# Kernel tuning notes

Measured on AMD Instinct MI355X. Metric: run time of the kernel, lower is better.

Reference implementation:

```python
import jax, jax.numpy as jnp
import numpy as np

CX, CY, FX, FY = 334.081, 169.808, 460.585, 460.268
EPS = 1e-07
T_ITER = 1000
MIN_POINTS = 5000
H, W, B = 360, 640, 2


def _point_cloud(depth_img):
    # depth_img: [C,H,W]; channel 2 if C==3 else channel 0
    depth = depth_img[2] if depth_img.shape[0] == 3 else depth_img[0]
    rows, cols = depth.shape
    c = jnp.arange(cols, dtype=depth.dtype)[None, :]
    r = jnp.arange(rows, dtype=depth.dtype)[:, None]
    valid = (depth > 0) & (depth < 65535)
    nanv = jnp.float32(jnp.nan)
    z = jnp.where(valid, depth / 1000.0, nanv)
    x = jnp.where(valid, z * (c - CX) / FX, nanv)
    y = jnp.where(valid, z * (r - CY) / FY, nanv)
    pcd = jnp.stack([x.ravel(), y.ravel(), z.ravel()], axis=1)  # [N,3]
    return pcd, valid.ravel()


def setup_inputs() -> dict:
    key = jax.random.key(0)
    k1, k2 = jax.random.split(key)
    fake = jax.random.uniform(k1, (B, 1, H, W), dtype=jnp.float32)
    real = jax.random.uniform(k2, (B, 1, H, W), dtype=jnp.float32)
    return {"fake": fake, "real": real, "epoch": 5, "show_image": 0}


def _forward(fake, real, epoch):
    real_pcd, vr = _point_cloud(real[0])
    fake_pcd, vf = _point_cloud(fake[0])
    real_pcd = real_pcd * 1000.0
    fake_pcd = fake_pcd * 1000.0
    # pcd[pcd==0] = eps  (NaN==0 is False, NaNs preserved)
    real_pcd = jnp.where(real_pcd == 0, EPS, real_pcd)
    fake_pcd = jnp.where(fake_pcd == 0, EPS, fake_pcd)

    # combined validity mask (real-valid then fake-valid filtering chain)
    m = vr & vf
    cnt = jnp.maximum(jnp.sum(m), 1)

    def sel(v, fill):
        return jnp.where(m, v, fill)

    def mrmse(a, b):
        d = sel(a, 0.0) - sel(b, 0.0)
        return jnp.sqrt(jnp.sum(d * d) / cnt)

    lossX = mrmse(real_pcd[:, 0], fake_pcd[:, 0])
    lossY = mrmse(real_pcd[:, 1], fake_pcd[:, 1])
    lossZ = mrmse(real_pcd[:, 2], fake_pcd[:, 2])
    dlog = jnp.log(jnp.abs(sel(real_pcd[:, 2], 1.0))) - jnp.log(jnp.abs(sel(fake_pcd[:, 2], 1.0)))
    RMSE_log = 10000.0 * jnp.sqrt(jnp.sum(jnp.where(m, dlog * dlog, 0.0)) / cnt)
    loss17 = RMSE_log * jnp.abs(10.0 * (3.0 - jnp.exp(lossX) - jnp.exp(lossY) - jnp.exp(lossZ)))

    # ---- batched RANSAC plane fit on normalized fake cloud ----
    nan_cloud = jnp.where(jnp.isnan(fake_pcd), 0.0, fake_pcd)
    pts = nan_cloud / jnp.max(nan_cloud)  # [N,3]
    N = pts.shape[0]
    thresh = jnp.maximum(jnp.float32(0.025 - 0.001 * epoch), jnp.float32(0.005))

    rkey = jax.random.key(42)
    idx = jax.random.randint(rkey, (T_ITER, 3), 0, N)  # 3 sample points per trial
    p = pts[idx]  # [T,3,3]
    vA = p[:, 1] - p[:, 0]
    vB = p[:, 2] - p[:, 0]
    nrm = jnp.cross(vA, vB)
    nrm = nrm / jnp.linalg.norm(nrm, axis=1, keepdims=True)  # unit normals [T,3]
    kk = -jnp.sum(nrm * p[:, 1], axis=1)  # plane offsets [T]
    dist = pts @ nrm.T + kk[None, :]  # [N,T], |n|=1 so no extra divide
    inl = jnp.abs(dist) <= thresh  # [N,T]
    counts = jnp.sum(inl, axis=0)  # [T]
    # keep first trial with strictly-largest count among counts > minPoints
    score = jnp.where(counts > MIN_POINTS, counts, -1)
    best = jnp.argmax(score)
    a, b, c, d = nrm[best, 0], nrm[best, 1], nrm[best, 2], kk[best]
    inlier_mask = inl[:, best]  # [N]

    # translation/rotation were built via torch.tensor(...) -> detached in torch
    trans = jax.lax.stop_gradient(jnp.stack([jnp.zeros(()), jnp.zeros(()), d / c]))
    n2 = a * a + b * b + c * c
    cos_t = c / jnp.sqrt(n2)
    sin_t = jnp.sqrt((a * a + b * b) / n2)
    sab = jnp.sqrt(a * a + b * b)
    u1 = b / sab
    u2 = -a / sab
    R = jnp.stack([
        jnp.stack([cos_t + u1 * u1 * (1 - cos_t), u1 * u2 * (1 - cos_t), u2 * sin_t]),
        jnp.stack([u1 * u2 * (1 - cos_t), cos_t + u2 * u2 * (1 - cos_t), -u1 * sin_t]),
        jnp.stack([-u2 * sin_t, u1 * sin_t, cos_t]),
    ])
    Rt = jax.lax.stop_gradient(R).T  # torch transposes before matmul

    plane_pts = pts + trans
    zc = (plane_pts @ Rt)[:, 2]  # rotated z for all points; inliers selected by mask
    icnt = jnp.maximum(jnp.sum(inlier_mask), 1)
    zmax = jnp.max(jnp.where(inlier_mask, zc, -jnp.inf))
    zmin = jnp.min(jnp.where(inlier_mask, zc, jnp.inf))
    below = jnp.sum(jnp.where(inlier_mask, jnp.abs(zc - zmax), 0.0)) / icnt
    above = jnp.sum(jnp.where(inlier_mask, jnp.abs(zc - zmin), 0.0)) / icnt
    above = jnp.where(above == 0, jnp.float32(1e-07), above)
    plane_mean_dist_grad = 1000.0 * (above + below)

    loss_curv = loss17 + plane_mean_dist_grad
    delta = jnp.stack([RMSE_log, lossX, lossY, lossZ, plane_mean_dist_grad, loss17])
    return delta, loss_curv


def reference(fake, real, epoch, show_image):
    del show_image  # unused in the loss math
    return _forward(fake, real, epoch)
```

## Files before the change

### kernel.cpp

```cpp
#include <hip/hip_runtime.h>

namespace {

typedef float v2f __attribute__((ext_vector_type(2)));

constexpr int kW = 640;
constexpr unsigned kSpan = 230400u;
constexpr int kB1 = 900;
constexpr int kB3 = 1024;
constexpr int kPPB3 = 225;
constexpr int kB5 = 900;
constexpr unsigned kPoison = 0xAAAAAAAAu;

constexpr size_t kOffMaxv    = 0;
constexpr size_t kOffL17     = 8;
constexpr size_t kOffSel     = 16;
constexpr size_t kOffC3      = 320;
constexpr size_t kOffC5      = 384;
constexpr size_t kOffPlanes  = 512;
constexpr size_t kOffSP      = 512 + 16384;
constexpr size_t kOffZP      = kOffSP + 43200;
constexpr size_t kOffPartial = kOffZP + 28800;
constexpr size_t kOffPts     = kOffPartial + (size_t)kB3 * 256 * 4;

__device__ __forceinline__ void ast64(unsigned long long* p, unsigned long long v) {
  __hip_atomic_store(p, v, __ATOMIC_RELAXED, __HIP_MEMORY_SCOPE_AGENT);
}
__device__ __forceinline__ unsigned long long ald64(const unsigned long long* p) {
  return __hip_atomic_load(p, __ATOMIC_RELAXED, __HIP_MEMORY_SCOPE_AGENT);
}
__device__ __forceinline__ void ast32(unsigned* p, unsigned v) {
  __hip_atomic_store(p, v, __ATOMIC_RELAXED, __HIP_MEMORY_SCOPE_AGENT);
}
__device__ __forceinline__ unsigned ald32(const unsigned* p) {
  return __hip_atomic_load(p, __ATOMIC_RELAXED, __HIP_MEMORY_SCOPE_AGENT);
}

__device__ __forceinline__ unsigned rotl32(unsigned v, int r) {
  return (v << r) | (v >> (32 - r));
}

__device__ __forceinline__ void threefry(unsigned c0, unsigned c1,
                                         unsigned& o0, unsigned& o1) {
  const unsigned ks0 = 0u, ks1 = 42u, ks2 = 0x1BD11BDAu ^ 0u ^ 42u;
  unsigned x0 = c0 + ks0, x1 = c1 + ks1;
#define TFR(r) { x0 += x1; x1 = rotl32(x1, (r)); x1 ^= x0; }
  TFR(13) TFR(15) TFR(26) TFR(6)
  x0 += ks1; x1 += ks2 + 1u;
  TFR(17) TFR(29) TFR(16) TFR(24)
  x0 += ks2; x1 += ks0 + 2u;
  TFR(13) TFR(15) TFR(26) TFR(6)
  x0 += ks0; x1 += ks1 + 3u;
  TFR(17) TFR(29) TFR(16) TFR(24)
  x0 += ks1; x1 += ks2 + 4u;
  TFR(13) TFR(15) TFR(26) TFR(6)
  x0 += ks2; x1 += ks0 + 5u;
#undef TFR
  o0 = x0; o1 = x1;
}

__device__ __forceinline__ void pix_coords(float d, int row, int col, bool& valid,
                                           float& x, float& y, float& z) {
  valid = (d > 0.0f) && (d < 65535.0f);
  float z0 = d / 1000.0f;
  float x0 = z0 * ((float)col - 334.081f) / 460.585f;
  float y0 = z0 * ((float)row - 169.808f) / 460.268f;
  x = x0 * 1000.0f;
  y = y0 * 1000.0f;
  z = z0 * 1000.0f;
  if (x == 0.0f) x = 1e-7f;
  if (y == 0.0f) y = 1e-7f;
  if (z == 0.0f) z = 1e-7f;
}

__device__ __forceinline__ void make_pt(float d, int row, int col, float maxv,
                                        float& x, float& y, float& z) {
  bool v; float a, b, c;
  pix_coords(d, row, col, v, a, b, c);
  x = (v ? a : 0.f) / maxv;
  y = (v ? b : 0.f) / maxv;
  z = (v ? c : 0.f) / maxv;
}

__device__ __forceinline__ float get_thresh(int ep) {
  return (float)fmax(0.025 - 0.001 * (double)ep, 0.005);
}

__global__ __launch_bounds__(256) void k_stats(const float* __restrict__ fake,
                                               const float* __restrict__ real,
                                               char* __restrict__ ws) {
  int* maxvBits = (int*)(ws + kOffMaxv);
  double* sp = (double*)(ws + kOffSP);
  float4* ptsraw = (float4*)(ws + kOffPts);

  const int b = blockIdx.x, t = threadIdx.x;
  const int lane = t & 63, wid = t >> 6;

  __shared__ double sD0[4], sD1[4], sD2[4], sD3[4];
  __shared__ int sI0[4];
  __shared__ float sF0[4];

  int i = b * 256 + t;
  int row = i / kW, col = i - row * kW;
  bool vr, vf; float rx, ry, rz, fx, fy, fz;
  pix_coords(real[i], row, col, vr, rx, ry, rz);
  pix_coords(fake[i], row, col, vf, fx, fy, fz);
  ptsraw[i] = make_float4(vf ? fx : 0.f, vf ? fy : 0.f, vf ? fz : 0.f, 0.f);
  double dx2 = 0, dy2 = 0, dz2 = 0, dl2 = 0; int cc = 0;
  if (vr && vf) {
    float ddx = rx - fx, ddy = ry - fy, ddz = rz - fz;
    dx2 = (double)ddx * (double)ddx;
    dy2 = (double)ddy * (double)ddy;
    dz2 = (double)ddz * (double)ddz;
    double dl = log(fabs((double)rz)) - log(fabs((double)fz));
    dl2 = dl * dl;
    cc = 1;
  }
  float mx = vf ? fmaxf(fmaxf(fx, fy), fz) : 0.0f;
  for (int o = 32; o; o >>= 1) {
    dx2 += __shfl_down(dx2, o); dy2 += __shfl_down(dy2, o);
    dz2 += __shfl_down(dz2, o); dl2 += __shfl_down(dl2, o);
    cc += __shfl_down(cc, o);
    mx = fmaxf(mx, __shfl_down(mx, o));
  }
  if (lane == 0) { sD0[wid]=dx2; sD1[wid]=dy2; sD2[wid]=dz2; sD3[wid]=dl2;
                   sI0[wid]=cc; sF0[wid]=mx; }
  __syncthreads();
  if (t == 0) {
    double* e = sp + (size_t)b * 6;
    e[0] = sD0[0]+sD0[1]+sD0[2]+sD0[3];
    e[1] = sD1[0]+sD1[1]+sD1[2]+sD1[3];
    e[2] = sD2[0]+sD2[1]+sD2[2]+sD2[3];
    e[3] = sD3[0]+sD3[1]+sD3[2]+sD3[3];
    e[4] = (double)(sI0[0]+sI0[1]+sI0[2]+sI0[3]);
    float bm = fmaxf(fmaxf(sF0[0], sF0[1]), fmaxf(sF0[2], sF0[3]));
    atomicMax(maxvBits, (int)__float_as_uint(bm));
  }
}

__global__ __launch_bounds__(256) void k_planes_scalars(const float* __restrict__ fake,
                                                        float* __restrict__ out,
                                                        char* __restrict__ ws) {
  const int* maxvBits = (const int*)(ws + kOffMaxv);
  double* loss17p = (double*)(ws + kOffL17);
  unsigned* selkeyp = (unsigned*)(ws + kOffSel);
  float4* planes = (float4*)(ws + kOffPlanes);
  const double* sp = (const double*)(ws + kOffSP);

  const int t = threadIdx.x;
  const int lane = t & 63, wid = t >> 6;

  if (blockIdx.x == 16) {
    __shared__ double sD0[4], sD1[4], sD2[4], sD3[4];
    __shared__ int sI0[4];
    double gx = 0, gy = 0, gz = 0, gl = 0; int gc = 0;
    for (int r = t; r < kB1; r += 256) {
      const double* e = sp + (size_t)r * 6;
      gx += e[0]; gy += e[1]; gz += e[2]; gl += e[3];
      gc += (int)e[4];
    }
    for (int o = 32; o; o >>= 1) {
      gx += __shfl_down(gx, o); gy += __shfl_down(gy, o);
      gz += __shfl_down(gz, o); gl += __shfl_down(gl, o);
      gc += __shfl_down(gc, o);
    }
    if (lane == 0) { sD0[wid]=gx; sD1[wid]=gy; sD2[wid]=gz; sD3[wid]=gl; sI0[wid]=gc; }
    __syncthreads();
    if (t == 0) {
      double SX = sD0[0]+sD0[1]+sD0[2]+sD0[3];
      double SY = sD1[0]+sD1[1]+sD1[2]+sD1[3];
      double SZ = sD2[0]+sD2[1]+sD2[2]+sD2[3];
      double SL = sD3[0]+sD3[1]+sD3[2]+sD3[3];
      int CN = sI0[0]+sI0[1]+sI0[2]+sI0[3];
      double cntd = (CN > 0) ? (double)CN : 1.0;
      double lossX = sqrt(SX / cntd);
      double lossY = sqrt(SY / cntd);
      double lossZ = sqrt(SZ / cntd);
      double rmse_log = 10000.0 * sqrt(SL / cntd);
      double loss17 = rmse_log * fabs(10.0 * (3.0 - exp(lossX) - exp(lossY) - exp(lossZ)));
      *loss17p = loss17;
      *selkeyp = 0u;
      out[0] = (float)rmse_log;
      out[1] = (float)lossX;
      out[2] = (float)lossY;
      out[3] = (float)lossZ;
      out[5] = (float)loss17;
    }
  } else {
    const float maxv = __uint_as_float((unsigned)*maxvBits);
    __shared__ float sX[192], sY[192], sZ[192];
    if (t < 192) {
      int j = t / 3;
      int v = t - j * 3;
      int pid = blockIdx.x * 64 + j;
      if (pid < 1000) {
        unsigned p = 3u * (unsigned)pid + (unsigned)v;
        unsigned o0, o1;
        threefry(p, p + 3000u, o0, o1);
        unsigned idx = o1 % kSpan;
        int row = (int)(idx / kW), col = (int)idx - row * kW;
        float x, y, z;
        make_pt(fake[idx], row, col, maxv, x, y, z);
        sX[t] = x; sY[t] = y; sZ[t] = z;
      }
    }
    __syncthreads();
    if (t < 64) {
      int pid = blockIdx.x * 64 + t;
      if (pid < 1000) {
        float px[3], py[3], pz[3];
#pragma unroll
        for (int v = 0; v < 3; v++) {
          px[v] = sX[3 * t + v]; py[v] = sY[3 * t + v]; pz[v] = sZ[3 * t + v];
        }
        float ax = px[1]-px[0], ay = py[1]-py[0], az = pz[1]-pz[0];
        float bx = px[2]-px[0], by = py[2]-py[0], bz = pz[2]-pz[0];
        float nx = ay*bz - az*by;
        float ny = az*bx - ax*bz;
        float nz = ax*by - ay*bx;
        float nn = sqrtf(nx*nx + ny*ny + nz*nz);
        nx /= nn; ny /= nn; nz /= nn;
        float kk = -(nx*px[1] + ny*py[1] + nz*pz[1]);
        planes[pid] = make_float4(nx, ny, nz, kk);
      } else {
        planes[pid] = make_float4(0.f, 0.f, 0.f, 3e38f);
      }
    }
  }
}

__global__ __launch_bounds__(256) void k_count(const int* __restrict__ epoch,
                                               char* __restrict__ ws) {
  unsigned* selkeyp = (unsigned*)(ws + kOffSel);
  unsigned* ctr = (unsigned*)(ws + kOffC3);
  const float4* planes = (const float4*)(ws + kOffPlanes);
  unsigned* partial = (unsigned*)(ws + kOffPartial);
  const float4* ptsraw = (const float4*)(ws + kOffPts);

  const int b = blockIdx.x, t = threadIdx.x;
  const float th = get_thresh(*epoch);
  const float maxv = __uint_as_float(*(const unsigned*)(ws + kOffMaxv));

  __shared__ float4 sPts[kPPB3];
  __shared__ uint4 sAcc[16][16];
  __shared__ unsigned sArr;

  if (t < kPPB3) {
    float4 r = ptsraw[b * kPPB3 + t];
    sPts[t] = make_float4(r.x / maxv, r.y / maxv, r.z / maxv, 0.f);
  }
  float4 p0 = planes[t * 4 + 0], p1 = planes[t * 4 + 1];
  float4 p2 = planes[t * 4 + 2], p3 = planes[t * 4 + 3];
  v2f Ax = {p0.x, p1.x}, Ay = {p0.y, p1.y}, Az = {p0.z, p1.z}, Aw = {p0.w, p1.w};
  v2f Bx = {p2.x, p3.x}, By = {p2.y, p3.y}, Bz = {p2.z, p3.z}, Bw = {p2.w, p3.w};
  __syncthreads();

  int c0 = 0, c1 = 0, c2 = 0, c3 = 0;
#pragma unroll 5
  for (int s = 0; s < kPPB3; ++s) {
    float4 q = sPts[s];
    v2f qx = {q.x, q.x}, qy = {q.y, q.y}, qz = {q.z, q.z};
    v2f dA = __builtin_elementwise_fma(qx, Ax,
             __builtin_elementwise_fma(qy, Ay,
             __builtin_elementwise_fma(qz, Az, Aw)));
    v2f dB = __builtin_elementwise_fma(qx, Bx,
             __builtin_elementwise_fma(qy, By,
             __builtin_elementwise_fma(qz, Bz, Bw)));
    c0 += (fabsf(dA.x) <= th) ? 1 : 0;
    c1 += (fabsf(dA.y) <= th) ? 1 : 0;
    c2 += (fabsf(dB.x) <= th) ? 1 : 0;
    c3 += (fabsf(dB.y) <= th) ? 1 : 0;
  }
  ast32(&partial[b * 256 + t],
        (unsigned)c0 | ((unsigned)c1 << 8) | ((unsigned)c2 << 16) | ((unsigned)c3 << 24));

  __syncthreads();
  if (t == 0)
    sArr = __hip_atomic_fetch_add(ctr, 1u, __ATOMIC_RELAXED, __HIP_MEMORY_SCOPE_AGENT);
  __syncthreads();
  unsigned ret = sArr;
  if (ret < kPoison + (unsigned)(kB3 - 16)) return;

  int r = (int)(ret - (kPoison + (unsigned)(kB3 - 16)));
  if (t == 0) {
    while (ald32(ctr) != kPoison + (unsigned)kB3) __builtin_amdgcn_s_sleep(2);
  }
  __syncthreads();

  int owner = r * 16 + (t & 15);
  int chunk = t >> 4;
  unsigned s0 = 0, s1 = 0, s2 = 0, s3 = 0;
  for (int row = chunk * 64; row < chunk * 64 + 64; ++row) {
    unsigned v = ald32(&partial[row * 256 + owner]);
    s0 += v & 0xFFu; s1 += (v >> 8) & 0xFFu;
    s2 += (v >> 16) & 0xFFu; s3 += (v >> 24) & 0xFFu;
  }
  sAcc[t & 15][chunk] = make_uint4(s0, s1, s2, s3);
  __syncthreads();

  unsigned mykey = 0u;
  if (t < 16) {
    unsigned t0 = 0, t1 = 0, t2 = 0, t3 = 0;
    for (int j = 0; j < 16; ++j) {
      uint4 v = sAcc[t][j];
      t0 += v.x; t1 += v.y; t2 += v.z; t3 += v.w;
    }
    unsigned tot[4] = {t0, t1, t2, t3};
    int pbase = (r * 16 + t) * 4;
#pragma unroll
    for (int k = 0; k < 4; ++k) {
      int p = pbase + k;
      if (p < 1000) {
        int score = ((int)tot[k] > 5000) ? (int)tot[k] : -1;
        unsigned key = ((unsigned)(score + 2) << 10) | (unsigned)(1023 - p);
        mykey = key > mykey ? key : mykey;
      }
    }
  }
  for (int o = 32; o; o >>= 1) {
    unsigned other = __shfl_down(mykey, o);
    mykey = other > mykey ? other : mykey;
  }
  if (t == 0) atomicMax(selkeyp, mykey);
}

__global__ __launch_bounds__(256) void k_zc(const int* __restrict__ epoch,
                                            float* __restrict__ out,
                                            char* __restrict__ ws) {
  const double* loss17p = (const double*)(ws + kOffL17);
  unsigned* ctr = (unsigned*)(ws + kOffC5);
  const float4* planes = (const float4*)(ws + kOffPlanes);
  unsigned long long* zp = (unsigned long long*)(ws + kOffZP);
  const float4* ptsraw = (const float4*)(ws + kOffPts);

  const int b = blockIdx.x, t = threadIdx.x;
  const int lane = t & 63, wid = t >> 6;
  const float th = get_thresh(*epoch);
  const float maxv = __uint_as_float(*(const unsigned*)(ws + kOffMaxv));

  unsigned selkey = *(const unsigned*)(ws + kOffSel);
  int best = 1023 - (int)(selkey & 1023u);
  float4 pl = planes[best];
  const float a = pl.x, bb = pl.y, c = pl.z, d = pl.w;
  float n2 = a * a + bb * bb + c * c;
  float cos_t = c / sqrtf(n2);
  float sin_t = sqrtf((a * a + bb * bb) / n2);
  float sab = sqrtf(a * a + bb * bb);
  float u1 = bb / sab, u2 = -a / sab;
  const float r0 = -u2 * sin_t, r1 = u1 * sin_t, r2 = cos_t, tz = d / c;

  __shared__ double sD0[4];
  __shared__ int sI0[4];
  __shared__ float sF0[4], sF1[4];
  __shared__ unsigned sArr;

  double sz = 0.0; int ic = 0; float zmx = -INFINITY, zmn = -INFINITY;
  {
    float4 rw = ptsraw[b * 256 + t];
    float qx = rw.x / maxv, qy = rw.y / maxv, qz = rw.z / maxv;
    float dist = fmaf(qx, a, fmaf(qy, bb, fmaf(qz, c, d)));
    if (fabsf(dist) <= th) {
      float zc = fmaf(qx, r0, fmaf(qy, r1, (qz + tz) * r2));
      sz = (double)zc; ic = 1; zmx = zc; zmn = -zc;
    }
  }
  for (int o = 32; o; o >>= 1) {
    sz += __shfl_down(sz, o); ic += __shfl_down(ic, o);
    zmx = fmaxf(zmx, __shfl_down(zmx, o));
    zmn = fmaxf(zmn, __shfl_down(zmn, o));
  }
  if (lane == 0) { sD0[wid] = sz; sI0[wid] = ic; sF0[wid] = zmx; sF1[wid] = zmn; }
  __syncthreads();
  if (t == 0) {
    unsigned long long* e = zp + (size_t)b * 4;
    ast64(e + 0, __double_as_longlong(sD0[0]+sD0[1]+sD0[2]+sD0[3]));
    ast64(e + 1, (unsigned long long)(sI0[0]+sI0[1]+sI0[2]+sI0[3]));
    float bmx = fmaxf(fmaxf(sF0[0], sF0[1]), fmaxf(sF0[2], sF0[3]));
    float bmn = fmaxf(fmaxf(sF1[0], sF1[1]), fmaxf(sF1[2], sF1[3]));
    ast64(e + 2, (unsigned long long)__float_as_uint(bmx) |
                 ((unsigned long long)__float_as_uint(bmn) << 32));
  }
  __syncthreads();
  if (t == 0)
    sArr = __hip_atomic_fetch_add(ctr, 1u, __ATOMIC_RELAXED, __HIP_MEMORY_SCOPE_AGENT);
  __syncthreads();
  if (sArr != kPoison + (unsigned)(kB5 - 1)) return;

  {
    double gs = 0.0; int gi = 0; float gmx = -INFINITY, gmn = -INFINITY;
    for (int r = t; r < kB5; r += 256) {
      const unsigned long long* e = zp + (size_t)r * 4;
      gs += __longlong_as_double(ald64(e + 0));
      gi += (int)ald64(e + 1);
      unsigned long long mm = ald64(e + 2);
      gmx = fmaxf(gmx, __uint_as_float((unsigned)(mm & 0xFFFFFFFFu)));
      gmn = fmaxf(gmn, __uint_as_float((unsigned)(mm >> 32)));
    }
    for (int o = 32; o; o >>= 1) {
      gs += __shfl_down(gs, o); gi += __shfl_down(gi, o);
      gmx = fmaxf(gmx, __shfl_down(gmx, o));
      gmn = fmaxf(gmn, __shfl_down(gmn, o));
    }
    if (lane == 0) { sD0[wid] = gs; sI0[wid] = gi; sF0[wid] = gmx; sF1[wid] = gmn; }
    __syncthreads();
    if (t == 0) {
      double S = sD0[0]+sD0[1]+sD0[2]+sD0[3];
      int IC = sI0[0]+sI0[1]+sI0[2]+sI0[3];
      float MX = fmaxf(fmaxf(sF0[0], sF0[1]), fmaxf(sF0[2], sF0[3]));
      float MN = fmaxf(fmaxf(sF1[0], sF1[1]), fmaxf(sF1[2], sF1[3]));
      double below = 0.0, above = 0.0;
      if (IC > 0) {
        double icd = (double)IC;
        double mean = S / icd;
        below = (double)MX - mean;
        above = mean - (double)(-MN);
      }
      if (above == 0.0) above = 1e-7;
      double pmdg = 1000.0 * (above + below);
      out[4] = (float)pmdg;
      out[6] = (float)(*loss17p + pmdg);
    }
  }
}

}

extern "C" void kernel_launch(void* const* d_in, const int* in_sizes, int n_in,
                              void* d_out, int out_size, void* d_ws, size_t ws_size,
                              hipStream_t stream) {
  (void)in_sizes; (void)n_in; (void)out_size; (void)ws_size;
  const float* fake = (const float*)d_in[0];
  const float* real = (const float*)d_in[1];
  const int* epoch = (const int*)d_in[2];
  float* out = (float*)d_out;
  char* ws = (char*)d_ws;

  k_stats<<<kB1, 256, 0, stream>>>(fake, real, ws);
  k_planes_scalars<<<17, 256, 0, stream>>>(fake, out, ws);
  k_count<<<kB3, 256, 0, stream>>>(epoch, ws);
  k_zc<<<kB5, 256, 0, stream>>>(epoch, out, ws);
}
```

Measured before the change: 129.8 us.

## Replace last-block atomic grid sync with separate select and final kernels

Removes the atomic arrival counters and the spin-wait tail in the count and z-statistics kernels. The final reductions move into new kernels, k_select and k_final, that rely on stream ordering instead. The count kernel now uses 1800 blocks of 128 points instead of 1024 blocks of 225, which spreads work more finely across CUs and shortens the loop per block. The trade is two extra kernel launches against dropping the serialized spin-wait and atomic traffic, plus no longer depending on the poison value in the workspace.

```diff
diff --git a/kernel.cpp b/kernel.cpp
--- a/kernel.cpp
+++ b/kernel.cpp
@@ -7,34 +7,19 @@
 constexpr int kW = 640;
 constexpr unsigned kSpan = 230400u;
 constexpr int kB1 = 900;
-constexpr int kB3 = 1024;
-constexpr int kPPB3 = 225;
+constexpr int kB3 = 1800;
+constexpr int kPPB3 = 128;
+constexpr int kChunk = 113;
 constexpr int kB5 = 900;
-constexpr unsigned kPoison = 0xAAAAAAAAu;
 
 constexpr size_t kOffMaxv    = 0;
 constexpr size_t kOffL17     = 8;
 constexpr size_t kOffSel     = 16;
-constexpr size_t kOffC3      = 320;
-constexpr size_t kOffC5      = 384;
 constexpr size_t kOffPlanes  = 512;
 constexpr size_t kOffSP      = 512 + 16384;
-constexpr size_t kOffZP      = kOffSP + 43200;
-constexpr size_t kOffPartial = kOffZP + 28800;
-constexpr size_t kOffPts     = kOffPartial + (size_t)kB3 * 256 * 4;
-
-__device__ __forceinline__ void ast64(unsigned long long* p, unsigned long long v) {
-  __hip_atomic_store(p, v, __ATOMIC_RELAXED, __HIP_MEMORY_SCOPE_AGENT);
-}
-__device__ __forceinline__ unsigned long long ald64(const unsigned long long* p) {
-  return __hip_atomic_load(p, __ATOMIC_RELAXED, __HIP_MEMORY_SCOPE_AGENT);
-}
-__device__ __forceinline__ void ast32(unsigned* p, unsigned v) {
-  __hip_atomic_store(p, v, __ATOMIC_RELAXED, __HIP_MEMORY_SCOPE_AGENT);
-}
-__device__ __forceinline__ unsigned ald32(const unsigned* p) {
-  return __hip_atomic_load(p, __ATOMIC_RELAXED, __HIP_MEMORY_SCOPE_AGENT);
-}
+constexpr size_t kOffZP      = 60416;
+constexpr size_t kOffPartial = 90112;
+constexpr size_t kOffPts     = 2097152;
 
 __device__ __forceinline__ unsigned rotl32(unsigned v, int r) {
   return (v << r) | (v >> (32 - r));
@@ -231,8 +216,6 @@
 
 __global__ __launch_bounds__(256) void k_count(const int* __restrict__ epoch,
                                                char* __restrict__ ws) {
-  unsigned* selkeyp = (unsigned*)(ws + kOffSel);
-  unsigned* ctr = (unsigned*)(ws + kOffC3);
   const float4* planes = (const float4*)(ws + kOffPlanes);
   unsigned* partial = (unsigned*)(ws + kOffPartial);
   const float4* ptsraw = (const float4*)(ws + kOffPts);
@@ -242,8 +225,6 @@
   const float maxv = __uint_as_float(*(const unsigned*)(ws + kOffMaxv));
 
   __shared__ float4 sPts[kPPB3];
-  __shared__ uint4 sAcc[16][16];
-  __shared__ unsigned sArr;
 
   if (t < kPPB3) {
     float4 r = ptsraw[b * kPPB3 + t];
@@ -256,7 +237,7 @@
   __syncthreads();
 
   int c0 = 0, c1 = 0, c2 = 0, c3 = 0;
-#pragma unroll 5
+#pragma unroll 4
   for (int s = 0; s < kPPB3; ++s) {
     float4 q = sPts[s];
     v2f qx = {q.x, q.x}, qy = {q.y, q.y}, qz = {q.z, q.z};
@@ -271,27 +252,26 @@
     c2 += (fabsf(dB.x) <= th) ? 1 : 0;
     c3 += (fabsf(dB.y) <= th) ? 1 : 0;
   }
-  ast32(&partial[b * 256 + t],
-        (unsigned)c0 | ((unsigned)c1 << 8) | ((unsigned)c2 << 16) | ((unsigned)c3 << 24));
-
-  __syncthreads();
-  if (t == 0)
-    sArr = __hip_atomic_fetch_add(ctr, 1u, __ATOMIC_RELAXED, __HIP_MEMORY_SCOPE_AGENT);
-  __syncthreads();
-  unsigned ret = sArr;
-  if (ret < kPoison + (unsigned)(kB3 - 16)) return;
-
-  int r = (int)(ret - (kPoison + (unsigned)(kB3 - 16)));
-  if (t == 0) {
-    while (ald32(ctr) != kPoison + (unsigned)kB3) __builtin_amdgcn_s_sleep(2);
-  }
-  __syncthreads();
+  partial[b * 256 + t] =
+      (unsigned)c0 | ((unsigned)c1 << 8) | ((unsigned)c2 << 16) | ((unsigned)c3 << 24);
+}
+
+__global__ __launch_bounds__(256) void k_select(char* __restrict__ ws) {
+  unsigned* selkeyp = (unsigned*)(ws + kOffSel);
+  const unsigned* partial = (const unsigned*)(ws + kOffPartial);
+
+  const int r = blockIdx.x;
+  const int t = threadIdx.x;
+
+  __shared__ uint4 sAcc[16][16];
 
   int owner = r * 16 + (t & 15);
   int chunk = t >> 4;
+  int rbeg = chunk * kChunk;
+  int rend = rbeg + kChunk; if (rend > kB3) rend = kB3;
   unsigned s0 = 0, s1 = 0, s2 = 0, s3 = 0;
-  for (int row = chunk * 64; row < chunk * 64 + 64; ++row) {
-    unsigned v = ald32(&partial[row * 256 + owner]);
+  for (int row = rbeg; row < rend; ++row) {
+    unsigned v = partial[row * 256 + owner];
     s0 += v & 0xFFu; s1 += (v >> 8) & 0xFFu;
     s2 += (v >> 16) & 0xFFu; s3 += (v >> 24) & 0xFFu;
   }
@@ -325,10 +305,7 @@
 }
 
 __global__ __launch_bounds__(256) void k_zc(const int* __restrict__ epoch,
-                                            float* __restrict__ out,
                                             char* __restrict__ ws) {
-  const double* loss17p = (const double*)(ws + kOffL17);
-  unsigned* ctr = (unsigned*)(ws + kOffC5);
   const float4* planes = (const float4*)(ws + kOffPlanes);
   unsigned long long* zp = (unsigned long long*)(ws + kOffZP);
   const float4* ptsraw = (const float4*)(ws + kOffPts);
@@ -352,7 +329,6 @@
   __shared__ double sD0[4];
   __shared__ int sI0[4];
   __shared__ float sF0[4], sF1[4];
-  __shared__ unsigned sArr;
 
   double sz = 0.0; int ic = 0; float zmx = -INFINITY, zmn = -INFINITY;
   {
@@ -373,53 +349,59 @@
   __syncthreads();
   if (t == 0) {
     unsigned long long* e = zp + (size_t)b * 4;
-    ast64(e + 0, __double_as_longlong(sD0[0]+sD0[1]+sD0[2]+sD0[3]));
-    ast64(e + 1, (unsigned long long)(sI0[0]+sI0[1]+sI0[2]+sI0[3]));
+    e[0] = __double_as_longlong(sD0[0]+sD0[1]+sD0[2]+sD0[3]);
+    e[1] = (unsigned long long)(sI0[0]+sI0[1]+sI0[2]+sI0[3]);
     float bmx = fmaxf(fmaxf(sF0[0], sF0[1]), fmaxf(sF0[2], sF0[3]));
     float bmn = fmaxf(fmaxf(sF1[0], sF1[1]), fmaxf(sF1[2], sF1[3]));
-    ast64(e + 2, (unsigned long long)__float_as_uint(bmx) |
-                 ((unsigned long long)__float_as_uint(bmn) << 32));
-  }
+    e[2] = (unsigned long long)__float_as_uint(bmx) |
+           ((unsigned long long)__float_as_uint(bmn) << 32);
+  }
+}
+
+__global__ __launch_bounds__(256) void k_final(float* __restrict__ out,
+                                               char* __restrict__ ws) {
+  const double* loss17p = (const double*)(ws + kOffL17);
+  const unsigned long long* zp = (const unsigned long long*)(ws + kOffZP);
+
+  const int t = threadIdx.x;
+  const int lane = t & 63, wid = t >> 6;
+
+  __shared__ double sD0[4];
+  __shared__ int sI0[4];
+  __shared__ float sF0[4], sF1[4];
+
+  double gs = 0.0; int gi = 0; float gmx = -INFINITY, gmn = -INFINITY;
+  for (int r = t; r < kB5; r += 256) {
+    const unsigned long long* e = zp + (size_t)r * 4;
+    gs += __longlong_as_double(e[0]);
+    gi += (int)e[1];
+    unsigned long long mm = e[2];
+    gmx = fmaxf(gmx, __uint_as_float((unsigned)(mm & 0xFFFFFFFFu)));
+    gmn = fmaxf(gmn, __uint_as_float((unsigned)(mm >> 32)));
+  }
+  for (int o = 32; o; o >>= 1) {
+    gs += __shfl_down(gs, o); gi += __shfl_down(gi, o);
+    gmx = fmaxf(gmx, __shfl_down(gmx, o));
+    gmn = fmaxf(gmn, __shfl_down(gmn, o));
+  }
+  if (lane == 0) { sD0[wid] = gs; sI0[wid] = gi; sF0[wid] = gmx; sF1[wid] = gmn; }
   __syncthreads();
-  if (t == 0)
-    sArr = __hip_atomic_fetch_add(ctr, 1u, __ATOMIC_RELAXED, __HIP_MEMORY_SCOPE_AGENT);
-  __syncthreads();
-  if (sArr != kPoison + (unsigned)(kB5 - 1)) return;
-
-  {
-    double gs = 0.0; int gi = 0; float gmx = -INFINITY, gmn = -INFINITY;
-    for (int r = t; r < kB5; r += 256) {
-      const unsigned long long* e = zp + (size_t)r * 4;
-      gs += __longlong_as_double(ald64(e + 0));
-      gi += (int)ald64(e + 1);
-      unsigned long long mm = ald64(e + 2);
-      gmx = fmaxf(gmx, __uint_as_float((unsigned)(mm & 0xFFFFFFFFu)));
-      gmn = fmaxf(gmn, __uint_as_float((unsigned)(mm >> 32)));
-    }
-    for (int o = 32; o; o >>= 1) {
-      gs += __shfl_down(gs, o); gi += __shfl_down(gi, o);
-      gmx = fmaxf(gmx, __shfl_down(gmx, o));
-      gmn = fmaxf(gmn, __shfl_down(gmn, o));
-    }
-    if (lane == 0) { sD0[wid] = gs; sI0[wid] = gi; sF0[wid] = gmx; sF1[wid] = gmn; }
-    __syncthreads();
-    if (t == 0) {
-      double S = sD0[0]+sD0[1]+sD0[2]+sD0[3];
-      int IC = sI0[0]+sI0[1]+sI0[2]+sI0[3];
-      float MX = fmaxf(fmaxf(sF0[0], sF0[1]), fmaxf(sF0[2], sF0[3]));
-      float MN = fmaxf(fmaxf(sF1[0], sF1[1]), fmaxf(sF1[2], sF1[3]));
-      double below = 0.0, above = 0.0;
-      if (IC > 0) {
-        double icd = (double)IC;
-        double mean = S / icd;
-        below = (double)MX - mean;
-        above = mean - (double)(-MN);
-      }
-      if (above == 0.0) above = 1e-7;
-      double pmdg = 1000.0 * (above + below);
-      out[4] = (float)pmdg;
-      out[6] = (float)(*loss17p + pmdg);
-    }
+  if (t == 0) {
+    double S = sD0[0]+sD0[1]+sD0[2]+sD0[3];
+    int IC = sI0[0]+sI0[1]+sI0[2]+sI0[3];
+    float MX = fmaxf(fmaxf(sF0[0], sF0[1]), fmaxf(sF0[2], sF0[3]));
+    float MN = fmaxf(fmaxf(sF1[0], sF1[1]), fmaxf(sF1[2], sF1[3]));
+    double below = 0.0, above = 0.0;
+    if (IC > 0) {
+      double icd = (double)IC;
+      double mean = S / icd;
+      below = (double)MX - mean;
+      above = mean - (double)(-MN);
+    }
+    if (above == 0.0) above = 1e-7;
+    double pmdg = 1000.0 * (above + below);
+    out[4] = (float)pmdg;
+    out[6] = (float)(*loss17p + pmdg);
   }
 }
 
@@ -438,5 +420,7 @@
   k_stats<<<kB1, 256, 0, stream>>>(fake, real, ws);
   k_planes_scalars<<<17, 256, 0, stream>>>(fake, out, ws);
   k_count<<<kB3, 256, 0, stream>>>(epoch, ws);
-  k_zc<<<kB5, 256, 0, stream>>>(epoch, out, ws);
-}
+  k_select<<<16, 256, 0, stream>>>(ws);
+  k_zc<<<kB5, 256, 0, stream>>>(epoch, ws);
+  k_final<<<1, 256, 0, stream>>>(out, ws);
+}
```

Result: slower. 136.5 us (+5.2%).
